# Kernel optimization log

Measured on AMD Instinct MI355X. Metric: run time of the kernel, lower is better.

The kernel has to match this reference:

```python
import jax, jax.numpy as jnp
import numpy as np

N_NODES = 50000
N_EDGES = 800000
IN_DIM = 128
EDGE_DIM = 32
HIDDEN = 128
NUM_LAYERS = 3
BN_EPS = 1e-5
RES_SCALE = 0.1


def setup_inputs() -> dict:
    key = jax.random.key(0)
    ks = jax.random.split(key, 10)
    x = jax.random.normal(ks[0], (N_NODES, IN_DIM), dtype=jnp.float32)
    edge_index = jax.random.randint(ks[1], (2, N_EDGES), 0, N_NODES, dtype=jnp.int64)
    edge_attr = jax.random.normal(ks[2], (N_EDGES, EDGE_DIM), dtype=jnp.float32)
    s = 0.05
    We = jax.random.normal(ks[3], (NUM_LAYERS, EDGE_DIM, HIDDEN), dtype=jnp.float32) * s
    be = jax.random.normal(ks[4], (NUM_LAYERS, HIDDEN), dtype=jnp.float32) * s
    W1 = jax.random.normal(ks[5], (NUM_LAYERS, HIDDEN, HIDDEN), dtype=jnp.float32) * s
    b1 = jax.random.normal(ks[6], (NUM_LAYERS, HIDDEN), dtype=jnp.float32) * s
    W2 = jax.random.normal(ks[7], (NUM_LAYERS, HIDDEN, HIDDEN), dtype=jnp.float32) * s
    b2 = jax.random.normal(ks[8], (NUM_LAYERS, HIDDEN), dtype=jnp.float32) * s
    gamma = jnp.ones((NUM_LAYERS, HIDDEN), dtype=jnp.float32)
    beta = jnp.zeros((NUM_LAYERS, HIDDEN), dtype=jnp.float32)
    return {"x": x, "edge_index": edge_index, "edge_attr": edge_attr,
            "We": We, "be": be, "W1": W1, "b1": b1, "W2": W2, "b2": b2,
            "gamma": gamma, "beta": beta}


def reference(x, edge_index, edge_attr, We, be, W1, b1, W2, b2, gamma, beta):
    # Dropout treated as eval-mode identity (deterministic reference).
    src = edge_index[0]  # x_j source nodes
    dst = edge_index[1]  # aggregation targets x_i
    n = x.shape[0]
    h = x
    for l in range(NUM_LAYERS):
        h_res = h
        # GINEConv message: ReLU(x_j + Linear(edge_attr)), eps=0
        e = edge_attr @ We[l] + be[l]            # [E, H]
        msg = jax.nn.relu(h[src] + e)            # [E, H]
        agg = jax.ops.segment_sum(msg, dst, num_segments=n)  # [N, H]
        z = h + agg                               # (1+eps)*x_i + sum, eps=0
        # GINE nn: Linear -> ReLU -> Linear
        z = jax.nn.relu(z @ W1[l] + b1[l]) @ W2[l] + b2[l]
        # BatchNorm over node axis (training batch stats)
        mu = jnp.mean(z, axis=0)
        var = jnp.var(z, axis=0)
        z = (z - mu) * jax.lax.rsqrt(var + BN_EPS) * gamma[l] + beta[l]
        z = jax.nn.relu(z)
        h = z + RES_SCALE * h_res
    return h
```

## Files before the change

### kernel.cpp

```cpp
#include <hip/hip_runtime.h>
#include <hip/hip_bf16.h>

#define N_NODES   50000
#define N_EDGES   800000
#define IN_DIM    128
#define EDGE_DIM  32
#define HIDDEN    128
#define NUM_LAYERS 3
#define BN_EPS    1e-5f
#define RES_SCALE 0.1f

typedef unsigned int   u32;
typedef unsigned short u16;
typedef _Float16 half2_t __attribute__((ext_vector_type(2)));
typedef _Float16 half8 __attribute__((ext_vector_type(8)));
typedef unsigned int u32x4 __attribute__((ext_vector_type(4)));
typedef float f32x4 __attribute__((ext_vector_type(4)));

#define AS4 __attribute__((address_space(4)))

__device__ __forceinline__ half2_t as_half2(u32 v) {
    union { u32 u; half2_t h; } c; c.u = v; return c.h;
}
__device__ __forceinline__ u32 pack_half2(float a, float b) {
    union { u32 u; half2_t h; } c;
    c.h.x = (_Float16)a; c.h.y = (_Float16)b; return c.u;
}

__global__ __launch_bounds__(256) void init_kernel(const float* __restrict__ x,
                                                   u32* __restrict__ h16,
                                                   u32* __restrict__ deg,
                                                   float* __restrict__ statsAll) {
    int idx = blockIdx.x * 256 + threadIdx.x;
    if (idx < N_NODES * 64) {
        int n = idx >> 6, w = idx & 63;
        int li = w >> 2, q = w & 3;
        int f = q * 16 + li;
        h16[idx] = pack_half2(x[n * HIDDEN + f], x[n * HIDDEN + 64 + f]);
    }
    if (idx < N_NODES) deg[idx] = 0u;
    if (idx < NUM_LAYERS * 256) statsAll[idx] = 0.f;
}

__global__ __launch_bounds__(256) void hist_kernel(const int* __restrict__ ei,
                                                   u32* __restrict__ deg) {
    int e = blockIdx.x * 256 + threadIdx.x;
    if (e < N_EDGES) atomicAdd(&deg[ei[N_EDGES + e]], 1u);
}

#define SCAN_NB ((N_NODES + 255) / 256)

__global__ __launch_bounds__(256) void scan1_kernel(const u32* __restrict__ deg,
                                                    u32* __restrict__ bsum) {
    int i = blockIdx.x * 256 + threadIdx.x;
    u32 v = (i < N_NODES) ? deg[i] : 0u;
    v += __shfl_down(v, 32, 64);
    v += __shfl_down(v, 16, 64);
    v += __shfl_down(v, 8, 64);
    v += __shfl_down(v, 4, 64);
    v += __shfl_down(v, 2, 64);
    v += __shfl_down(v, 1, 64);
    __shared__ u32 ws[4];
    if ((threadIdx.x & 63) == 0) ws[threadIdx.x >> 6] = v;
    __syncthreads();
    if (threadIdx.x == 0) bsum[blockIdx.x] = ws[0] + ws[1] + ws[2] + ws[3];
}

__global__ __launch_bounds__(256) void scan2_kernel(const u32* __restrict__ bsum,
                                                    u32* __restrict__ bbase,
                                                    u32* __restrict__ off) {
    __shared__ u32 tmp[256];
    int t = threadIdx.x;
    u32 v = (t < SCAN_NB) ? bsum[t] : 0u;
    tmp[t] = v;
    __syncthreads();
    for (int d = 1; d < 256; d <<= 1) {
        u32 u = (t >= d) ? tmp[t - d] : 0u;
        __syncthreads();
        tmp[t] += u;
        __syncthreads();
    }
    if (t < SCAN_NB) bbase[t] = (t == 0) ? 0u : tmp[t - 1];
    if (t == 255) off[N_NODES] = tmp[255];
}

__global__ __launch_bounds__(256) void scan3_kernel(const u32* __restrict__ deg,
                                                    const u32* __restrict__ bbase,
                                                    u32* __restrict__ off,
                                                    u32* __restrict__ cursor) {
    __shared__ u32 tmp[256];
    int t = threadIdx.x;
    int i = blockIdx.x * 256 + t;
    u32 v = (i < N_NODES) ? deg[i] : 0u;
    tmp[t] = v;
    __syncthreads();
    for (int d = 1; d < 256; d <<= 1) {
        u32 u = (t >= d) ? tmp[t - d] : 0u;
        __syncthreads();
        tmp[t] += u;
        __syncthreads();
    }
    if (i < N_NODES) {
        u32 excl = bbase[blockIdx.x] + tmp[t] - v;
        off[i] = excl;
        cursor[i] = excl;
    }
}

__global__ __launch_bounds__(256) void scatter_kernel(const int* __restrict__ ei,
                                                      u32* __restrict__ cursor,
                                                      int* __restrict__ ssrc,
                                                      const float* __restrict__ ea,
                                                      _Float16* __restrict__ ea_perm) {
    int e = blockIdx.x * 256 + threadIdx.x;
    if (e >= N_EDGES) return;
    int dst = ei[N_EDGES + e];
    u32 pos = atomicAdd(&cursor[dst], 1u);
    ssrc[pos] = ei[e];
    const float4* src = (const float4*)(ea + (size_t)e * EDGE_DIM);
    u32 buf[16];
#pragma unroll
    for (int q = 0; q < 8; q++) {
        float4 v = src[q];
        buf[2 * q + 0] = pack_half2(v.x, v.y);
        buf[2 * q + 1] = pack_half2(v.z, v.w);
    }
    uint4* dp = (uint4*)(ea_perm + (size_t)pos * EDGE_DIM);
#pragma unroll
    for (int q = 0; q < 4; q++)
        dp[q] = make_uint4(buf[4 * q], buf[4 * q + 1], buf[4 * q + 2], buf[4 * q + 3]);
}

__global__ __launch_bounds__(256) void wconv_kernel(const float* __restrict__ W1,
                                                    const float* __restrict__ W2,
                                                    const float* __restrict__ We,
                                                    _Float16* __restrict__ w1t,
                                                    _Float16* __restrict__ w2t,
                                                    _Float16* __restrict__ weT) {
    int idx = blockIdx.x * 256 + threadIdx.x;
    if (idx < NUM_LAYERS * 128 * 128) {
        int kk = idx & 127, f = (idx >> 7) & 127, l = idx >> 14;
        int w = kk >> 1;
        int k1 = 32 * (w >> 4) + (w & 15) + ((kk & 1) << 4);
        w1t[idx] = (_Float16)W1[l * 16384 + k1 * 128 + f];
        w2t[idx] = (_Float16)W2[l * 16384 + kk * 128 + f];
    }
    if (idx < NUM_LAYERS * 8 * 64) {
        int lane = idx & 63, c = (idx >> 6) & 7, l = idx >> 9;
        int rg = lane >> 4, li = lane & 15;
        _Float16* dst = weT + (size_t)idx * 8;
#pragma unroll
        for (int j = 0; j < 8; j++)
            dst[j] = (_Float16)We[l * (EDGE_DIM * HIDDEN) + (8 * rg + j) * HIDDEN + c * 16 + li];
    }
}

__global__ __launch_bounds__(256) void agg_mfma_kernel(
    const u32* __restrict__ h16p, const _Float16* __restrict__ ea_perm,
    const int* __restrict__ ssrc, const u32* __restrict__ off,
    const _Float16* __restrict__ weT, const float* __restrict__ be,
    u32* __restrict__ z16b) {
    int t = threadIdx.x, l = t & 63, li = l & 15, rg = l >> 4;

    half8 bfrag[8];
    const uint4* wp = (const uint4*)weT;
#pragma unroll
    for (int c = 0; c < 8; c++) {
        union { uint4 u; half8 h; } cv;
        cv.u = wp[c * 64 + l];
        bfrag[c] = cv.h;
    }
    float beC[8];
#pragma unroll
    for (int c = 0; c < 8; c++) beC[c] = be[c * 16 + li];

    const AS4 u32* coff = (const AS4 u32*)(unsigned long long)off;

    int wid = __builtin_amdgcn_readfirstlane(t >> 6);
    int slot = blockIdx.x * 4 + wid;
    int nslots = gridDim.x * 4;
    for (int n = slot; n < N_NODES; n += nslots) {
        int e0 = (int)coff[n], e1 = (int)coff[n + 1];
        f32x4 acc[8];
#pragma unroll
        for (int c = 0; c < 8; c++) acc[c] = (f32x4){0.f, 0.f, 0.f, 0.f};

        for (int et = e0; et < e1; et += 16) {
            union { uint4 u; half8 h; } av;
            av.u = *(const uint4*)(ea_perm + (size_t)(et + li) * 32 + rg * 8);
            f32x4 d[8];
#pragma unroll
            for (int c = 0; c < 8; c++) {
                f32x4 ci = (f32x4){beC[c], beC[c], beC[c], beC[c]};
                d[c] = __builtin_amdgcn_mfma_f32_16x16x32_f16(av.h, bfrag[c], ci, 0, 0, 0);
            }
            int eb = et + 4 * rg;
            if (et + 16 <= e1) {
                int s0 = ssrc[eb], s1 = ssrc[eb + 1], s2 = ssrc[eb + 2], s3 = ssrc[eb + 3];
                uint4 g0 = *(const uint4*)(h16p + (size_t)s0 * 64 + li * 4);
                uint4 g1 = *(const uint4*)(h16p + (size_t)s1 * 64 + li * 4);
                uint4 g2 = *(const uint4*)(h16p + (size_t)s2 * 64 + li * 4);
                uint4 g3 = *(const uint4*)(h16p + (size_t)s3 * 64 + li * 4);
                const uint4 g[4] = {g0, g1, g2, g3};
#pragma unroll
                for (int r = 0; r < 4; r++) {
                    u32 w0 = (&g[r].x)[0], w1 = (&g[r].x)[1];
                    u32 w2 = (&g[r].x)[2], w3 = (&g[r].x)[3];
                    acc[0][r] += fmaxf(d[0][r] + (float)as_half2(w0).x, 0.f);
                    acc[4][r] += fmaxf(d[4][r] + (float)as_half2(w0).y, 0.f);
                    acc[1][r] += fmaxf(d[1][r] + (float)as_half2(w1).x, 0.f);
                    acc[5][r] += fmaxf(d[5][r] + (float)as_half2(w1).y, 0.f);
                    acc[2][r] += fmaxf(d[2][r] + (float)as_half2(w2).x, 0.f);
                    acc[6][r] += fmaxf(d[6][r] + (float)as_half2(w2).y, 0.f);
                    acc[3][r] += fmaxf(d[3][r] + (float)as_half2(w3).x, 0.f);
                    acc[7][r] += fmaxf(d[7][r] + (float)as_half2(w3).y, 0.f);
                }
            } else {
                int sv[4];
                bool vd[4];
#pragma unroll
                for (int r = 0; r < 4; r++) {
                    int ee = eb + r;
                    int s = ssrc[ee];
                    vd[r] = (ee < e1);
                    sv[r] = vd[r] ? s : 0;
                }
#pragma unroll
                for (int r = 0; r < 4; r++) {
                    uint4 g = *(const uint4*)(h16p + (size_t)sv[r] * 64 + li * 4);
                    u32 w0 = g.x, w1 = g.y, w2 = g.z, w3 = g.w;
                    float m0 = fmaxf(d[0][r] + (float)as_half2(w0).x, 0.f);
                    float m4 = fmaxf(d[4][r] + (float)as_half2(w0).y, 0.f);
                    float m1 = fmaxf(d[1][r] + (float)as_half2(w1).x, 0.f);
                    float m5 = fmaxf(d[5][r] + (float)as_half2(w1).y, 0.f);
                    float m2 = fmaxf(d[2][r] + (float)as_half2(w2).x, 0.f);
                    float m6 = fmaxf(d[6][r] + (float)as_half2(w2).y, 0.f);
                    float m3 = fmaxf(d[3][r] + (float)as_half2(w3).x, 0.f);
                    float m7 = fmaxf(d[7][r] + (float)as_half2(w3).y, 0.f);
                    if (vd[r]) {
                        acc[0][r] += m0; acc[1][r] += m1; acc[2][r] += m2; acc[3][r] += m3;
                        acc[4][r] += m4; acc[5][r] += m5; acc[6][r] += m6; acc[7][r] += m7;
                    }
                }
            }
        }

        float s[8];
#pragma unroll
        for (int c = 0; c < 8; c++) {
            float v = acc[c][0] + acc[c][1] + acc[c][2] + acc[c][3];
            v += __shfl_xor(v, 16);
            v += __shfl_xor(v, 32);
            s[c] = v;
        }
        float x0 = (rg & 1) ? s[2] : s[0];
        float x1 = (rg & 1) ? s[6] : s[4];
        float va = (rg & 2) ? x1 : x0;
        float y0 = (rg & 1) ? s[3] : s[1];
        float y1 = (rg & 1) ? s[7] : s[5];
        float vb = (rg & 2) ? y1 : y0;
        const u32* hp = h16p + (size_t)n * 64 + li * 4 + 2 * (rg & 1);
        u32 ga = hp[0], gb = hp[1];
        float hva = (rg >= 2) ? (float)as_half2(ga).y : (float)as_half2(ga).x;
        float hvb = (rg >= 2) ? (float)as_half2(gb).y : (float)as_half2(gb).x;
        z16b[(size_t)n * 64 + l] = pack_half2(hva + va, hvb + vb);
    }
}

__global__ __launch_bounds__(256) void mlp_mfma_kernel(
    const u32* __restrict__ z16,
    const _Float16* __restrict__ w1t, const float* __restrict__ b1_,
    const _Float16* __restrict__ w2t, const float* __restrict__ b2_,
    float* __restrict__ z2, float* __restrict__ stats) {
    __shared__ __align__(16) char lds[65536];
    char* zh = lds;
    char* wh = lds + 32768;
    int t = threadIdx.x, l = t & 63, w = t >> 6;
    int li = l & 15, rg = l >> 4;
    int base = blockIdx.x * 128;

#pragma unroll
    for (int rep = 0; rep < 8; rep++) {
        int c = t + rep * 256;
        int n = c >> 4, s = c & 15;
        int gn = base + n;
        uint4 v = make_uint4(0u, 0u, 0u, 0u);
        if (gn < N_NODES) v = *(const uint4*)(z16 + (size_t)gn * 64 + s * 4);
        *(uint4*)(zh + n * 256 + ((s ^ (n & 7)) << 4)) = v;
    }
#pragma unroll
    for (int rep = 0; rep < 8; rep++) {
        int c = t + rep * 256;
        int f = c >> 4, s = c & 15;
        uint4 v = *(const uint4*)((const char*)w1t + f * 256 + s * 16);
        *(uint4*)(wh + f * 256 + ((s ^ (f & 7)) << 4)) = v;
    }
    __syncthreads();

    int f0 = w * 32 + li;
    int f1 = w * 32 + 16 + li;

    f32x4 acc0[8], acc1[8];
    {
        float bva = b1_[f0], bvb = b1_[f1];
#pragma unroll
        for (int m = 0; m < 8; m++) {
            acc0[m] = (f32x4){bva, bva, bva, bva};
            acc1[m] = (f32x4){bvb, bvb, bvb, bvb};
        }
    }
#pragma unroll
    for (int kt = 0; kt < 4; kt++) {
        int s = kt * 4 + rg;
        half8 bf0 = *(const half8*)(wh + f0 * 256 + ((s ^ (f0 & 7)) << 4));
        half8 bf1 = *(const half8*)(wh + f1 * 256 + ((s ^ (f1 & 7)) << 4));
#pragma unroll
        for (int m = 0; m < 8; m++) {
            int n = m * 16 + li;
            half8 af = *(const half8*)(zh + n * 256 + ((s ^ (n & 7)) << 4));
            acc0[m] = __builtin_amdgcn_mfma_f32_16x16x32_f16(af, bf0, acc0[m], 0, 0, 0);
            acc1[m] = __builtin_amdgcn_mfma_f32_16x16x32_f16(af, bf1, acc1[m], 0, 0, 0);
        }
    }
    __syncthreads();

#pragma unroll
    for (int m = 0; m < 8; m++) {
#pragma unroll
        for (int r = 0; r < 4; r++) {
            int n = m * 16 + rg * 4 + r;
            int s0 = f0 >> 3;
            *(_Float16*)(zh + n * 256 + ((s0 ^ (n & 7)) << 4) + (f0 & 7) * 2) =
                (_Float16)fmaxf(acc0[m][r], 0.f);
            int s1 = f1 >> 3;
            *(_Float16*)(zh + n * 256 + ((s1 ^ (n & 7)) << 4) + (f1 & 7) * 2) =
                (_Float16)fmaxf(acc1[m][r], 0.f);
        }
    }
#pragma unroll
    for (int rep = 0; rep < 8; rep++) {
        int c = t + rep * 256;
        int f = c >> 4, s = c & 15;
        uint4 v = *(const uint4*)((const char*)w2t + f * 256 + s * 16);
        *(uint4*)(wh + f * 256 + ((s ^ (f & 7)) << 4)) = v;
    }
    __syncthreads();

    {
        float cva = b2_[f0], cvb = b2_[f1];
#pragma unroll
        for (int m = 0; m < 8; m++) {
            acc0[m] = (f32x4){cva, cva, cva, cva};
            acc1[m] = (f32x4){cvb, cvb, cvb, cvb};
        }
    }
#pragma unroll
    for (int kt = 0; kt < 4; kt++) {
        int s = kt * 4 + rg;
        half8 bf0 = *(const half8*)(wh + f0 * 256 + ((s ^ (f0 & 7)) << 4));
        half8 bf1 = *(const half8*)(wh + f1 * 256 + ((s ^ (f1 & 7)) << 4));
#pragma unroll
        for (int m = 0; m < 8; m++) {
            int n = m * 16 + li;
            half8 af = *(const half8*)(zh + n * 256 + ((s ^ (n & 7)) << 4));
            acc0[m] = __builtin_amdgcn_mfma_f32_16x16x32_f16(af, bf0, acc0[m], 0, 0, 0);
            acc1[m] = __builtin_amdgcn_mfma_f32_16x16x32_f16(af, bf1, acc1[m], 0, 0, 0);
        }
    }

    float s0 = 0.f, q0 = 0.f, s1 = 0.f, q1 = 0.f;
#pragma unroll
    for (int m = 0; m < 8; m++) {
#pragma unroll
        for (int r = 0; r < 4; r++) {
            int gn = base + m * 16 + rg * 4 + r;
            if (gn < N_NODES) {
                float v0 = acc0[m][r], v1 = acc1[m][r];
                z2[(size_t)gn * 128 + f0] = v0;
                z2[(size_t)gn * 128 + f1] = v1;
                s0 += v0; q0 = fmaf(v0, v0, q0);
                s1 += v1; q1 = fmaf(v1, v1, q1);
            }
        }
    }
    s0 += __shfl_xor(s0, 16); s0 += __shfl_xor(s0, 32);
    q0 += __shfl_xor(q0, 16); q0 += __shfl_xor(q0, 32);
    s1 += __shfl_xor(s1, 16); s1 += __shfl_xor(s1, 32);
    q1 += __shfl_xor(q1, 16); q1 += __shfl_xor(q1, 32);
    if (rg == 0) {
        unsafeAtomicAdd(&stats[f0], s0);
        unsafeAtomicAdd(&stats[128 + f0], q0);
        unsafeAtomicAdd(&stats[f1], s1);
        unsafeAtomicAdd(&stats[128 + f1], q1);
    }
}

__global__ __launch_bounds__(256) void bn_kernel(
    const float* __restrict__ z2, const float* __restrict__ stats,
    const float* __restrict__ gamma, const float* __restrict__ beta,
    u32* __restrict__ h16, float* __restrict__ out, int write_out) {
    int idx = blockIdx.x * 256 + threadIdx.x;
    if (idx >= N_NODES * 64) return;
    int n = idx >> 6, w = idx & 63;
    int li = w >> 2, q = w & 3;
    int f = q * 16 + li, fh = f + 64;
    const float inv_n = 1.0f / (float)N_NODES;
    float mu_l = stats[f] * inv_n;
    float mu_h = stats[fh] * inv_n;
    float var_l = stats[HIDDEN + f] * inv_n - mu_l * mu_l;
    float var_h = stats[HIDDEN + fh] * inv_n - mu_h * mu_h;
    float inv_l = rsqrtf(var_l + BN_EPS);
    float inv_h = rsqrtf(var_h + BN_EPS);
    float zl = (z2[n * HIDDEN + f]  - mu_l) * inv_l * gamma[f]  + beta[f];
    float zh = (z2[n * HIDDEN + fh] - mu_h) * inv_h * gamma[fh] + beta[fh];
    zl = fmaxf(zl, 0.f);
    zh = fmaxf(zh, 0.f);
    half2_t hh = as_half2(h16[idx]);
    float hn_l = fmaf(RES_SCALE, (float)hh.x, zl);
    float hn_h = fmaf(RES_SCALE, (float)hh.y, zh);
    h16[idx] = pack_half2(hn_l, hn_h);
    if (write_out) {
        out[n * HIDDEN + f]  = hn_l;
        out[n * HIDDEN + fh] = hn_h;
    }
}

extern "C" void kernel_launch(void* const* d_in, const int* in_sizes, int n_in,
                              void* d_out, int out_size, void* d_ws, size_t ws_size,
                              hipStream_t stream) {
    const float* x     = (const float*)d_in[0];
    const int*   ei    = (const int*)d_in[1];
    const float* ea    = (const float*)d_in[2];
    const float* We    = (const float*)d_in[3];
    const float* be    = (const float*)d_in[4];
    const float* W1    = (const float*)d_in[5];
    const float* b1    = (const float*)d_in[6];
    const float* W2    = (const float*)d_in[7];
    const float* b2    = (const float*)d_in[8];
    const float* gamma = (const float*)d_in[9];
    const float* beta  = (const float*)d_in[10];
    float* out = (float*)d_out;

    char* wsp = (char*)d_ws;
    const size_t NH = (size_t)N_NODES * HIDDEN;
    u32*      h16    = (u32*)wsp;      wsp += (size_t)N_NODES * 64 * 4;
    u32*      z16    = (u32*)wsp;      wsp += (size_t)N_NODES * 64 * 4;
    float*    z2     = (float*)wsp;    wsp += NH * 4;
    _Float16* ea_perm= (_Float16*)wsp; wsp += (size_t)N_EDGES * EDGE_DIM * 2;
    _Float16* w1t    = (_Float16*)wsp; wsp += (size_t)NUM_LAYERS * 128 * 128 * 2;
    _Float16* w2t    = (_Float16*)wsp; wsp += (size_t)NUM_LAYERS * 128 * 128 * 2;
    _Float16* weT    = (_Float16*)wsp; wsp += (size_t)NUM_LAYERS * 4096 * 2;
    float*    statsA = (float*)wsp;    wsp += (size_t)NUM_LAYERS * 256 * 4;
    u32*      deg    = (u32*)wsp;      wsp += (size_t)N_NODES * 4;
    u32*      cursor = (u32*)wsp;      wsp += (size_t)N_NODES * 4;
    int*      ssrc   = (int*)wsp;      wsp += (size_t)N_EDGES * 4;
    u32*      off    = (u32*)wsp;      wsp += (size_t)(N_NODES + 1) * 4;
    u32*      bsum   = (u32*)wsp;      wsp += (size_t)SCAN_NB * 4;
    u32*      bbase  = (u32*)wsp;      wsp += (size_t)SCAN_NB * 4;

    const int p_blocks  = (N_NODES * 64 + 255) / 256;
    const int e_blocks  = (N_EDGES + 255) / 256;
    const int m_blocks  = (N_NODES + 127) / 128;
    const int w_blocks  = (NUM_LAYERS * 128 * 128 + 255) / 256;

    init_kernel<<<p_blocks, 256, 0, stream>>>(x, h16, deg, statsA);
    hist_kernel<<<e_blocks, 256, 0, stream>>>(ei, deg);
    scan1_kernel<<<SCAN_NB, 256, 0, stream>>>(deg, bsum);
    scan2_kernel<<<1, 256, 0, stream>>>(bsum, bbase, off);
    scan3_kernel<<<SCAN_NB, 256, 0, stream>>>(deg, bbase, off, cursor);
    scatter_kernel<<<e_blocks, 256, 0, stream>>>(ei, cursor, ssrc, ea, ea_perm);
    wconv_kernel<<<w_blocks, 256, 0, stream>>>(W1, W2, We, w1t, w2t, weT);

    for (int l = 0; l < NUM_LAYERS; l++) {
        agg_mfma_kernel<<<4096, 256, 0, stream>>>(
            h16, ea_perm, ssrc, off,
            weT + (size_t)l * 4096, be + (size_t)l * HIDDEN, z16);
        mlp_mfma_kernel<<<m_blocks, 256, 0, stream>>>(
            z16, w1t + (size_t)l * 16384, b1 + (size_t)l * HIDDEN,
            w2t + (size_t)l * 16384, b2 + (size_t)l * HIDDEN,
            z2, statsA + (size_t)l * 256);
        bn_kernel<<<p_blocks, 256, 0, stream>>>(
            z2, statsA + (size_t)l * 256, gamma + (size_t)l * HIDDEN, beta + (size_t)l * HIDDEN,
            h16, out, (l == NUM_LAYERS - 1) ? 1 : 0);
    }
}
```

Before: 679.0 us.

## Software-pipeline edge gathers across nodes in aggregation with contiguous node chunks per wave

```diff
diff --git a/kernel.cpp b/kernel.cpp
--- a/kernel.cpp
+++ b/kernel.cpp
@@ -155,6 +155,33 @@
     }
 }
 
+__device__ __forceinline__ void agg_epilogue(int node, const f32x4* __restrict__ acc,
+                                             const u32* __restrict__ h16p,
+                                             u32* __restrict__ z16b,
+                                             int li, int rg, int l) {
+    float s[8];
+#pragma unroll
+    for (int c = 0; c < 8; c++) {
+        float v = acc[c][0] + acc[c][1] + acc[c][2] + acc[c][3];
+        v += __shfl_xor(v, 16);
+        v += __shfl_xor(v, 32);
+        s[c] = v;
+    }
+    float x0 = (rg & 1) ? s[2] : s[0];
+    float x1 = (rg & 1) ? s[6] : s[4];
+    float va = (rg & 2) ? x1 : x0;
+    float y0 = (rg & 1) ? s[3] : s[1];
+    float y1 = (rg & 1) ? s[7] : s[5];
+    float vb = (rg & 2) ? y1 : y0;
+    const u32* hp = h16p + (size_t)node * 64 + li * 4 + 2 * (rg & 1);
+    u32 ga = hp[0], gb = hp[1];
+    float hva = (rg >= 2) ? (float)as_half2(ga).y : (float)as_half2(ga).x;
+    float hvb = (rg >= 2) ? (float)as_half2(gb).y : (float)as_half2(gb).x;
+    z16b[(size_t)node * 64 + l] = pack_half2(hva + va, hvb + vb);
+}
+
+#define AGG_NPW 4
+#define AGG_SLOTS ((N_NODES + AGG_NPW - 1) / AGG_NPW)
 __global__ __launch_bounds__(256) void agg_mfma_kernel(
     const u32* __restrict__ h16p, const _Float16* __restrict__ ea_perm,
     const int* __restrict__ ssrc, const u32* __restrict__ off,
@@ -178,92 +205,94 @@
 
     int wid = __builtin_amdgcn_readfirstlane(t >> 6);
     int slot = blockIdx.x * 4 + wid;
-    int nslots = gridDim.x * 4;
-    for (int n = slot; n < N_NODES; n += nslots) {
-        int e0 = (int)coff[n], e1 = (int)coff[n + 1];
-        f32x4 acc[8];
-#pragma unroll
-        for (int c = 0; c < 8; c++) acc[c] = (f32x4){0.f, 0.f, 0.f, 0.f};
-
-        for (int et = e0; et < e1; et += 16) {
-            union { uint4 u; half8 h; } av;
-            av.u = *(const uint4*)(ea_perm + (size_t)(et + li) * 32 + rg * 8);
-            f32x4 d[8];
-#pragma unroll
-            for (int c = 0; c < 8; c++) {
-                f32x4 ci = (f32x4){beC[c], beC[c], beC[c], beC[c]};
-                d[c] = __builtin_amdgcn_mfma_f32_16x16x32_f16(av.h, bfrag[c], ci, 0, 0, 0);
+    if (slot >= AGG_SLOTS) return;
+    int na = slot * AGG_NPW;
+    int nb = na + AGG_NPW; if (nb > N_NODES) nb = N_NODES;
+
+    f32x4 acc[8];
+#pragma unroll
+    for (int c = 0; c < 8; c++) acc[c] = (f32x4){0.f, 0.f, 0.f, 0.f};
+
+    int n = na;
+    int e0 = (int)coff[n], e1 = (int)coff[n + 1];
+    while (e0 == e1) {
+        agg_epilogue(n, acc, h16p, z16b, li, rg, l);
+        n++;
+        if (n >= nb) return;
+        e0 = e1; e1 = (int)coff[n + 1];
+    }
+    int et = e0;
+    int eb = et + 4 * rg;
+    int sv0 = ssrc[(eb + 0 < e1) ? eb + 0 : et];
+    int sv1 = ssrc[(eb + 1 < e1) ? eb + 1 : et];
+    int sv2 = ssrc[(eb + 2 < e1) ? eb + 2 : et];
+    int sv3 = ssrc[(eb + 3 < e1) ? eb + 3 : et];
+    uint4 Af = *(const uint4*)(ea_perm + (size_t)(et + li) * 32 + rg * 8);
+    uint4 g0 = *(const uint4*)(h16p + (size_t)sv0 * 64 + li * 4);
+    uint4 g1 = *(const uint4*)(h16p + (size_t)sv1 * 64 + li * 4);
+    uint4 g2 = *(const uint4*)(h16p + (size_t)sv2 * 64 + li * 4);
+    uint4 g3 = *(const uint4*)(h16p + (size_t)sv3 * 64 + li * 4);
+
+    while (true) {
+        int etn = et + 16;
+        int n2 = n, et2 = 0, e12 = 0;
+        bool more;
+        if (etn < e1) { et2 = etn; e12 = e1; more = true; }
+        else {
+            n2 = n + 1; more = false;
+            if (n2 < nb) {
+                int a = e1, b = (int)coff[n2 + 1];
+                while (a == b && n2 + 1 < nb) { n2++; a = b; b = (int)coff[n2 + 1]; }
+                if (a < b) { et2 = a; e12 = b; more = true; }
             }
-            int eb = et + 4 * rg;
-            if (et + 16 <= e1) {
-                int s0 = ssrc[eb], s1 = ssrc[eb + 1], s2 = ssrc[eb + 2], s3 = ssrc[eb + 3];
-                uint4 g0 = *(const uint4*)(h16p + (size_t)s0 * 64 + li * 4);
-                uint4 g1 = *(const uint4*)(h16p + (size_t)s1 * 64 + li * 4);
-                uint4 g2 = *(const uint4*)(h16p + (size_t)s2 * 64 + li * 4);
-                uint4 g3 = *(const uint4*)(h16p + (size_t)s3 * 64 + li * 4);
-                const uint4 g[4] = {g0, g1, g2, g3};
-#pragma unroll
-                for (int r = 0; r < 4; r++) {
-                    u32 w0 = (&g[r].x)[0], w1 = (&g[r].x)[1];
-                    u32 w2 = (&g[r].x)[2], w3 = (&g[r].x)[3];
-                    acc[0][r] += fmaxf(d[0][r] + (float)as_half2(w0).x, 0.f);
-                    acc[4][r] += fmaxf(d[4][r] + (float)as_half2(w0).y, 0.f);
-                    acc[1][r] += fmaxf(d[1][r] + (float)as_half2(w1).x, 0.f);
-                    acc[5][r] += fmaxf(d[5][r] + (float)as_half2(w1).y, 0.f);
-                    acc[2][r] += fmaxf(d[2][r] + (float)as_half2(w2).x, 0.f);
-                    acc[6][r] += fmaxf(d[6][r] + (float)as_half2(w2).y, 0.f);
-                    acc[3][r] += fmaxf(d[3][r] + (float)as_half2(w3).x, 0.f);
-                    acc[7][r] += fmaxf(d[7][r] + (float)as_half2(w3).y, 0.f);
-                }
-            } else {
-                int sv[4];
-                bool vd[4];
-#pragma unroll
-                for (int r = 0; r < 4; r++) {
-                    int ee = eb + r;
-                    int s = ssrc[ee];
-                    vd[r] = (ee < e1);
-                    sv[r] = vd[r] ? s : 0;
-                }
-#pragma unroll
-                for (int r = 0; r < 4; r++) {
-                    uint4 g = *(const uint4*)(h16p + (size_t)sv[r] * 64 + li * 4);
-                    u32 w0 = g.x, w1 = g.y, w2 = g.z, w3 = g.w;
-                    float m0 = fmaxf(d[0][r] + (float)as_half2(w0).x, 0.f);
-                    float m4 = fmaxf(d[4][r] + (float)as_half2(w0).y, 0.f);
-                    float m1 = fmaxf(d[1][r] + (float)as_half2(w1).x, 0.f);
-                    float m5 = fmaxf(d[5][r] + (float)as_half2(w1).y, 0.f);
-                    float m2 = fmaxf(d[2][r] + (float)as_half2(w2).x, 0.f);
-                    float m6 = fmaxf(d[6][r] + (float)as_half2(w2).y, 0.f);
-                    float m3 = fmaxf(d[3][r] + (float)as_half2(w3).x, 0.f);
-                    float m7 = fmaxf(d[7][r] + (float)as_half2(w3).y, 0.f);
-                    if (vd[r]) {
-                        acc[0][r] += m0; acc[1][r] += m1; acc[2][r] += m2; acc[3][r] += m3;
-                        acc[4][r] += m4; acc[5][r] += m5; acc[6][r] += m6; acc[7][r] += m7;
-                    }
-                }
+        }
+        int st0 = 0, st1 = 0, st2 = 0, st3 = 0;
+        uint4 A2 = Af;
+        if (more) {
+            int eb2 = et2 + 4 * rg;
+            st0 = ssrc[(eb2 + 0 < e12) ? eb2 + 0 : et2];
+            st1 = ssrc[(eb2 + 1 < e12) ? eb2 + 1 : et2];
+            st2 = ssrc[(eb2 + 2 < e12) ? eb2 + 2 : et2];
+            st3 = ssrc[(eb2 + 3 < e12) ? eb2 + 3 : et2];
+            A2 = *(const uint4*)(ea_perm + (size_t)(et2 + li) * 32 + rg * 8);
+        }
+        {
+            union { uint4 u; half8 h; } av; av.u = Af;
+            int ebase = et + 4 * rg;
+            bool v0 = (ebase + 0) < e1, v1 = (ebase + 1) < e1;
+            bool v2 = (ebase + 2) < e1, v3 = (ebase + 3) < e1;
+#pragma unroll
+            for (int q = 0; q < 4; q++) {
+                f32x4 cl = (f32x4){beC[q], beC[q], beC[q], beC[q]};
+                f32x4 ch = (f32x4){beC[q + 4], beC[q + 4], beC[q + 4], beC[q + 4]};
+                f32x4 dl = __builtin_amdgcn_mfma_f32_16x16x32_f16(av.h, bfrag[q], cl, 0, 0, 0);
+                f32x4 dh = __builtin_amdgcn_mfma_f32_16x16x32_f16(av.h, bfrag[q + 4], ch, 0, 0, 0);
+                u32 w0 = (&g0.x)[q], w1 = (&g1.x)[q], w2 = (&g2.x)[q], w3 = (&g3.x)[q];
+                float m;
+                m = fmaxf(dl[0] + (float)as_half2(w0).x, 0.f); acc[q][0]     += v0 ? m : 0.f;
+                m = fmaxf(dh[0] + (float)as_half2(w0).y, 0.f); acc[q + 4][0] += v0 ? m : 0.f;
+                m = fmaxf(dl[1] + (float)as_half2(w1).x, 0.f); acc[q][1]     += v1 ? m : 0.f;
+                m = fmaxf(dh[1] + (float)as_half2(w1).y, 0.f); acc[q + 4][1] += v1 ? m : 0.f;
+                m = fmaxf(dl[2] + (float)as_half2(w2).x, 0.f); acc[q][2]     += v2 ? m : 0.f;
+                m = fmaxf(dh[2] + (float)as_half2(w2).y, 0.f); acc[q + 4][2] += v2 ? m : 0.f;
+                m = fmaxf(dl[3] + (float)as_half2(w3).x, 0.f); acc[q][3]     += v3 ? m : 0.f;
+                m = fmaxf(dh[3] + (float)as_half2(w3).y, 0.f); acc[q + 4][3] += v3 ? m : 0.f;
             }
         }
-
-        float s[8];
-#pragma unroll
-        for (int c = 0; c < 8; c++) {
-            float v = acc[c][0] + acc[c][1] + acc[c][2] + acc[c][3];
-            v += __shfl_xor(v, 16);
-            v += __shfl_xor(v, 32);
-            s[c] = v;
-        }
-        float x0 = (rg & 1) ? s[2] : s[0];
-        float x1 = (rg & 1) ? s[6] : s[4];
-        float va = (rg & 2) ? x1 : x0;
-        float y0 = (rg & 1) ? s[3] : s[1];
-        float y1 = (rg & 1) ? s[7] : s[5];
-        float vb = (rg & 2) ? y1 : y0;
-        const u32* hp = h16p + (size_t)n * 64 + li * 4 + 2 * (rg & 1);
-        u32 ga = hp[0], gb = hp[1];
-        float hva = (rg >= 2) ? (float)as_half2(ga).y : (float)as_half2(ga).x;
-        float hvb = (rg >= 2) ? (float)as_half2(gb).y : (float)as_half2(gb).x;
-        z16b[(size_t)n * 64 + l] = pack_half2(hva + va, hvb + vb);
+        if (etn >= e1) {
+            agg_epilogue(n, acc, h16p, z16b, li, rg, l);
+#pragma unroll
+            for (int c = 0; c < 8; c++) acc[c] = (f32x4){0.f, 0.f, 0.f, 0.f};
+            int mend = more ? n2 : nb;
+            for (int m = n + 1; m < mend; m++)
+                agg_epilogue(m, acc, h16p, z16b, li, rg, l);
+        }
+        if (!more) break;
+        g0 = *(const uint4*)(h16p + (size_t)st0 * 64 + li * 4);
+        g1 = *(const uint4*)(h16p + (size_t)st1 * 64 + li * 4);
+        g2 = *(const uint4*)(h16p + (size_t)st2 * 64 + li * 4);
+        g3 = *(const uint4*)(h16p + (size_t)st3 * 64 + li * 4);
+        Af = A2; n = n2; et = et2; e1 = e12;
     }
 }
 
@@ -461,6 +490,7 @@
     const int p_blocks  = (N_NODES * 64 + 255) / 256;
     const int e_blocks  = (N_EDGES + 255) / 256;
     const int m_blocks  = (N_NODES + 127) / 128;
+    const int a_blocks  = (AGG_SLOTS + 3) / 4;
     const int w_blocks  = (NUM_LAYERS * 128 * 128 + 255) / 256;
 
     init_kernel<<<p_blocks, 256, 0, stream>>>(x, h16, deg, statsA);
@@ -472,7 +502,7 @@
     wconv_kernel<<<w_blocks, 256, 0, stream>>>(W1, W2, We, w1t, w2t, weT);
 
     for (int l = 0; l < NUM_LAYERS; l++) {
-        agg_mfma_kernel<<<4096, 256, 0, stream>>>(
+        agg_mfma_kernel<<<a_blocks, 256, 0, stream>>>(
             h16, ea_perm, ssrc, off,
             weT + (size_t)l * 4096, be + (size_t)l * HIDDEN, z16);
         mlp_mfma_kernel<<<m_blocks, 256, 0, stream>>>(
```

New measurement: 600.5 us. 1.13x faster.
